# Optimization experiments

Hardware: AMD Instinct MI355X
Metric: run time of the kernel (lower is better)

## Reference

```python
import jax, jax.numpy as jnp
import numpy as np

B, T = 512, 512
VOCAB, EMB, DEC = 30001, 512, 128
MAX_OOVS = 50


def setup_inputs() -> dict:
    key = jax.random.key(0)
    ks = jax.random.split(key, 24)
    rn = lambda k, shp, s=0.05: (jax.random.normal(k, shp, dtype=jnp.float32) * s)
    emb = rn(ks[0], (VOCAB, EMB), 1.0).at[0].set(0.0)  # padding_idx=0
    return {
        'h_i': jax.random.normal(ks[1], (B, T, DEC), dtype=jnp.float32),
        'h_prev': jax.random.normal(ks[2], (B, DEC), dtype=jnp.float32),
        'c_prev': jax.random.normal(ks[3], (B, DEC), dtype=jnp.float32),
        'context_vector': jax.random.normal(ks[4], (B, DEC), dtype=jnp.float32),
        'coverage': jax.random.uniform(ks[5], (B, T), dtype=jnp.float32),
        'emb': emb,
        'W_ih': rn(ks[6], (4 * DEC, EMB)), 'W_hh': rn(ks[7], (4 * DEC, DEC)),
        'b_ih': rn(ks[8], (4 * DEC,)), 'b_hh': rn(ks[9], (4 * DEC,)),
        'W1_w': rn(ks[10], (EMB, EMB + DEC)), 'W1_b': rn(ks[11], (EMB,)),
        'W2_w': rn(ks[12], (1, 3 * DEC + EMB)), 'W2_b': rn(ks[13], (1,)),
        'V1_w': rn(ks[14], (3 * DEC, 2 * DEC)), 'V1_b': rn(ks[15], (3 * DEC,)),
        'V2_w': rn(ks[16], (VOCAB, 3 * DEC)), 'V2_b': rn(ks[17], (VOCAB,)),
        'Wh_w': rn(ks[18], (DEC, DEC)),
        'Ws_w': rn(ks[19], (DEC, 2 * DEC)), 'Ws_b': rn(ks[20], (DEC,)),
        'Wc_w': rn(ks[21], (DEC, 1)),
        'V_w': rn(ks[22], (1, DEC)),
        'x': jax.random.randint(ks[23], (B, 1), 0, VOCAB),
        'code_ext': jax.random.randint(jax.random.fold_in(key, 99), (B, T), 0, VOCAB + MAX_OOVS),
        'max_oovs': MAX_OOVS,
    }


def reference(h_i, h_prev, c_prev, context_vector, coverage, emb,
              W_ih, W_hh, b_ih, b_hh, W1_w, W1_b, W2_w, W2_b,
              V1_w, V1_b, V2_w, V2_b, Wh_w, Ws_w, Ws_b, Wc_w, V_w,
              x, code_ext, max_oovs):
    xe = emb[x[:, 0]]                                        # [B, EMB]
    x1 = jnp.concatenate([xe, context_vector], 1) @ W1_w.T + W1_b
    # LSTMCell (gate order i, f, g, o)
    gates = x1 @ W_ih.T + b_ih + h_prev @ W_hh.T + b_hh
    i, f, g, o = jnp.split(gates, 4, axis=1)
    c = jax.nn.sigmoid(f) * c_prev + jax.nn.sigmoid(i) * jnp.tanh(g)
    h = jax.nn.sigmoid(o) * jnp.tanh(c)
    s_t = jnp.concatenate([h, c], 1)                         # [B, 2*DEC]
    # Bahdanau attention with coverage
    enc_f = h_i @ Wh_w.T                                     # [B, T, DEC]
    dec_f = (s_t @ Ws_w.T + Ws_b)[:, None, :]
    cov_f = coverage[:, :, None] * Wc_w[:, 0][None, None, :]
    e_t = jnp.tanh(enc_f + dec_f + cov_f) @ V_w[0]           # [B, T]
    a_t = jax.nn.softmax(e_t, axis=-1)
    coverage_new = coverage + a_t
    ctx = jnp.einsum('bt,btd->bd', a_t, h_i)                 # [B, DEC]
    # vocab distribution
    pv = jnp.concatenate([h, ctx], 1) @ V1_w.T + V1_b
    pv = jax.nn.softmax(pv @ V2_w.T + V2_b, axis=1)          # [B, VOCAB]
    p_gen = jax.nn.sigmoid(jnp.concatenate([ctx, s_t, xe], 1) @ W2_w.T + W2_b)  # [B,1]
    pv = p_gen * pv
    attn_dist = (1.0 - p_gen) * a_t
    pv_ext = jnp.concatenate([pv, jnp.zeros((pv.shape[0], max_oovs), pv.dtype)], axis=-1)
    rows = jnp.arange(pv.shape[0])[:, None]
    final_dist = pv_ext.at[rows, code_ext].add(attn_dist)    # scatter_add copy mechanism
    return (final_dist, attn_dist, h, c, coverage_new, ctx)
```

## Files before the change

kernel.cpp:

```cpp
#include <hip/hip_runtime.h>
#include <math.h>

#define B_    512
#define T_    512
#define DEC_  128
#define EMB_  512
#define VOC_  30001
#define VEXT_ 30051

typedef float f32x4 __attribute__((ext_vector_type(4)));
typedef short s16x4 __attribute__((ext_vector_type(4)));
typedef short s16x8 __attribute__((ext_vector_type(8)));
typedef unsigned u32x4 __attribute__((ext_vector_type(4)));

#define L2E 1.4426950408889634f

__device__ __forceinline__ float sigmoid_f(float x) {
  return __builtin_amdgcn_rcpf(1.f + exp2f(-x * L2E));
}
__device__ __forceinline__ float tanh_f(float x) {
  return 1.f - 2.f * __builtin_amdgcn_rcpf(exp2f(x * (2.f * L2E)) + 1.f);
}
__device__ __forceinline__ short f2bf(float f) {
  unsigned u = __builtin_bit_cast(unsigned, f);
  u += 0x7FFFu + ((u >> 16) & 1u);
  return (short)(u >> 16);
}
__device__ __forceinline__ float bf2f(unsigned short h) {
  return __builtin_bit_cast(float, (unsigned)h << 16);
}
__device__ __forceinline__ float bitsf(unsigned u) {
  return __builtin_bit_cast(float, u);
}
__device__ __forceinline__ unsigned pk_bf16(float lo, float hi) {
  unsigned r;
  asm("v_cvt_pk_bf16_f32 %0, %1, %2" : "=v"(r) : "v"(lo), "v"(hi));
  return r;
}
__device__ __forceinline__ s16x8 pk8(f32x4 w0, f32x4 w1) {
  u32x4 r;
  r[0] = pk_bf16(w0[0], w0[1]); r[1] = pk_bf16(w0[2], w0[3]);
  r[2] = pk_bf16(w1[0], w1[1]); r[3] = pk_bf16(w1[2], w1[3]);
  return __builtin_bit_cast(s16x8, r);
}
__device__ __forceinline__ unsigned short* logit_row(float* outF, int b) {
  size_t byteoff = ((size_t)b * VEXT_ * 4 + 127) & ~(size_t)127;
  return (unsigned short*)((char*)outF + byteoff);
}
__device__ __forceinline__ void gload_lds16(const void* g, void* l) {
  __builtin_amdgcn_global_load_lds(
      (const __attribute__((address_space(1))) void*)g,
      (__attribute__((address_space(3))) void*)l, 16, 0, 0);
}

__global__ __launch_bounds__(256) void k0_prep32(
    const float* __restrict__ Whw, unsigned short* __restrict__ bw) {
  const int t = threadIdx.x;
#pragma unroll
  for (int i = 0; i < 8; ++i) {
    int p = t + 256 * i;
    int f = p >> 6, l = p & 63;
    int nf = f >> 2, kf = f & 3;
    int row = nf * 16 + (l & 15);
    int col = kf * 32 + (l >> 4) * 8;
    const float* src = Whw + row * 128 + col;
    f32x4 w0 = *(const f32x4*)src;
    f32x4 w1 = *(const f32x4*)(src + 4);
    *(s16x8*)&bw[p * 8] = pk8(w0, w1);
  }
}

__global__ __launch_bounds__(256) void k0b_prepv2h(
    const float* __restrict__ V2w, unsigned short* __restrict__ v2bh) {
  int p = blockIdx.x * 256 + threadIdx.x;
  int row = p / 48;
  int k = (p - row * 48) * 8;
  s16x8 bb;
  if (row < VOC_) {
    const float* src = V2w + (size_t)row * 384 + k;
    f32x4 w0 = *(const f32x4*)src;
    f32x4 w1 = *(const f32x4*)(src + 4);
    bb = pk8(w0, w1);
  } else {
    bb = (s16x8){0, 0, 0, 0, 0, 0, 0, 0};
  }
  *(s16x8*)&v2bh[(size_t)p * 8] = bb;
}

__global__ __launch_bounds__(256) void k0c_prepv1(
    const float* __restrict__ V1w, unsigned short* __restrict__ v1bh) {
  int p = blockIdx.x * 256 + threadIdx.x;
  int row = p >> 5, k = (p & 31) * 8;
  const float* src = V1w + row * 256 + k;
  *(s16x8*)&v1bh[p * 8] = pk8(*(const f32x4*)src, *(const f32x4*)(src + 4));
}

__global__ __launch_bounds__(256) void k1_x1(
    const float* __restrict__ emb, const int* __restrict__ x,
    const float* __restrict__ ctxp, const float* __restrict__ W1w,
    const float* __restrict__ W1b, float* __restrict__ x1) {
  __shared__ float As[32][33];
  __shared__ float Ws[32][33];
  const int tid = threadIdx.x;
  const int f0 = blockIdx.x * 32, b0 = blockIdx.y * 32;
  const int row = tid >> 3, seg = tid & 7;
  const int tx = tid & 15, ty = tid >> 4;
  float a00 = 0.f, a01 = 0.f, a10 = 0.f, a11 = 0.f;
  for (int k0 = 0; k0 < 640; k0 += 32) {
    int k = k0 + seg * 4;
    f32x4 av;
    if (k < 512) {
      int xb = x[b0 + row];
      av = *(const f32x4*)(emb + xb * 512 + k);
    } else {
      av = *(const f32x4*)(ctxp + (b0 + row) * 128 + (k - 512));
    }
    As[row][seg * 4 + 0] = av[0]; As[row][seg * 4 + 1] = av[1];
    As[row][seg * 4 + 2] = av[2]; As[row][seg * 4 + 3] = av[3];
    f32x4 wv = *(const f32x4*)(W1w + (f0 + row) * 640 + k);
    Ws[row][seg * 4 + 0] = wv[0]; Ws[row][seg * 4 + 1] = wv[1];
    Ws[row][seg * 4 + 2] = wv[2]; Ws[row][seg * 4 + 3] = wv[3];
    __syncthreads();
#pragma unroll
    for (int kk = 0; kk < 32; ++kk) {
      float v0 = As[ty * 2][kk], v1 = As[ty * 2 + 1][kk];
      float w0 = Ws[tx * 2][kk], w1 = Ws[tx * 2 + 1][kk];
      a00 += v0 * w0; a01 += v0 * w1; a10 += v1 * w0; a11 += v1 * w1;
    }
    __syncthreads();
  }
  int fo = f0 + tx * 2, bo = b0 + ty * 2;
  x1[bo * 512 + fo]           = a00 + W1b[fo];
  x1[bo * 512 + fo + 1]       = a01 + W1b[fo + 1];
  x1[(bo + 1) * 512 + fo]     = a10 + W1b[fo];
  x1[(bo + 1) * 512 + fo + 1] = a11 + W1b[fo + 1];
}

__global__ __launch_bounds__(256) void k2_gates(
    const float* __restrict__ x1, const float* __restrict__ hprev,
    const float* __restrict__ Wih, const float* __restrict__ Whh,
    const float* __restrict__ bih, const float* __restrict__ bhh,
    float* __restrict__ gates) {
  __shared__ float As[32][33];
  __shared__ float Ws[32][33];
  const int tid = threadIdx.x;
  const int f0 = blockIdx.x * 32, b0 = blockIdx.y * 32;
  const int row = tid >> 3, seg = tid & 7;
  const int tx = tid & 15, ty = tid >> 4;
  float a00 = 0.f, a01 = 0.f, a10 = 0.f, a11 = 0.f;
  for (int k0 = 0; k0 < 640; k0 += 32) {
    int k = k0 + seg * 4;
    f32x4 av, wv;
    if (k < 512) {
      av = *(const f32x4*)(x1 + (b0 + row) * 512 + k);
      wv = *(const f32x4*)(Wih + (f0 + row) * 512 + k);
    } else {
      av = *(const f32x4*)(hprev + (b0 + row) * 128 + (k - 512));
      wv = *(const f32x4*)(Whh + (f0 + row) * 128 + (k - 512));
    }
    As[row][seg * 4 + 0] = av[0]; As[row][seg * 4 + 1] = av[1];
    As[row][seg * 4 + 2] = av[2]; As[row][seg * 4 + 3] = av[3];
    Ws[row][seg * 4 + 0] = wv[0]; Ws[row][seg * 4 + 1] = wv[1];
    Ws[row][seg * 4 + 2] = wv[2]; Ws[row][seg * 4 + 3] = wv[3];
    __syncthreads();
#pragma unroll
    for (int kk = 0; kk < 32; ++kk) {
      float v0 = As[ty * 2][kk], v1 = As[ty * 2 + 1][kk];
      float w0 = Ws[tx * 2][kk], w1 = Ws[tx * 2 + 1][kk];
      a00 += v0 * w0; a01 += v0 * w1; a10 += v1 * w0; a11 += v1 * w1;
    }
    __syncthreads();
  }
  int fo = f0 + tx * 2, bo = b0 + ty * 2;
  gates[bo * 512 + fo]           = a00 + bih[fo] + bhh[fo];
  gates[bo * 512 + fo + 1]       = a01 + bih[fo + 1] + bhh[fo + 1];
  gates[(bo + 1) * 512 + fo]     = a10 + bih[fo] + bhh[fo];
  gates[(bo + 1) * 512 + fo + 1] = a11 + bih[fo + 1] + bhh[fo + 1];
}

__global__ __launch_bounds__(128) void k3_lstm(
    const float* __restrict__ gates, const float* __restrict__ cprev,
    const float* __restrict__ Wsw, const float* __restrict__ Wsb,
    float* __restrict__ out_h, float* __restrict__ out_c,
    float* __restrict__ decf, unsigned short* __restrict__ hc_bf) {
  __shared__ float st[256];
  int b = blockIdx.x, d = threadIdx.x;
  const float* g = gates + b * 512;
  float iv = sigmoid_f(g[d]);
  float fv = sigmoid_f(g[128 + d]);
  float gv = tanh_f(g[256 + d]);
  float ov = sigmoid_f(g[384 + d]);
  float c = fv * cprev[b * 128 + d] + iv * gv;
  float h = ov * tanh_f(c);
  out_h[b * 128 + d] = h;
  out_c[b * 128 + d] = c;
  hc_bf[b * 256 + d] = (unsigned short)f2bf(h);
  st[d] = h; st[128 + d] = c;
  __syncthreads();
  float acc = Wsb[d];
  const float* wr = Wsw + d * 256;
#pragma unroll 4
  for (int k = 0; k < 256; ++k) acc += st[k] * wr[k];
  decf[b * 128 + d] = acc;
}

__global__ __launch_bounds__(512) void k45_attn(
    const float* __restrict__ h_i, const unsigned short* __restrict__ bw,
    const float* __restrict__ decf, const float* __restrict__ cov,
    const float* __restrict__ Wcw, const float* __restrict__ Vw,
    float* __restrict__ a_t, float* __restrict__ cov_out,
    float* __restrict__ ctx_out, unsigned short* __restrict__ hc_bf) {
  __shared__ unsigned short whl[16384];
  __shared__ float sm[512];
  __shared__ float red[8][128];
  __shared__ float wred[8];
  __shared__ float dls[128], vls[128], wls[128];
  const int b = blockIdx.x;
  const int tid = threadIdx.x;
  const int wv = tid >> 6, lane = tid & 63;
  const int lm = lane & 15, lg = lane >> 4;
  const int t0w = wv * 64;

#pragma unroll
  for (int i = 0; i < 4; ++i)
    gload_lds16(&bw[(tid + i * 512) * 8], &whl[(tid + i * 512) * 8]);
  if (tid < 128) {
    dls[tid] = decf[b * 128 + tid];
    vls[tid] = Vw[tid];
    wls[tid] = Wcw[tid];
  }
  __syncthreads();

  const volatile float* vlp = vls;
  const volatile float* dlp = dls;
  const volatile float* wlp = wls;
  float E1 = 0.f;
#pragma unroll
  for (int nf = 0; nf < 8; ++nf) E1 += fabsf(vlp[nf * 16 + lm]);
  E1 += __shfl_xor(E1, 1); E1 += __shfl_xor(E1, 2);
  E1 += __shfl_xor(E1, 4); E1 += __shfl_xor(E1, 8);

  const f32x4 zf4 = {0.f, 0.f, 0.f, 0.f};
  const float* abase = h_i + ((size_t)(b * 512 + t0w + lm)) * 128 + lg * 8;

  f32x4 r0, r1, r2, r3, r4, r5, r6, r7;
  f32x4 cv_raw;
  f32x4 c0 = zf4, c1 = zf4, c2 = zf4, c3 = zf4;
  f32x4 c4 = zf4, c5 = zf4, c6 = zf4, c7 = zf4;
#define K45_LOADC(c)                                            \
  do {                                                          \
    const float* p_ = abase + (size_t)(c) * 16 * 128;           \
    r0 = *(const f32x4*)(p_ + 0);   r1 = *(const f32x4*)(p_ + 4);   \
    r2 = *(const f32x4*)(p_ + 32);  r3 = *(const f32x4*)(p_ + 36);  \
    r4 = *(const f32x4*)(p_ + 64);  r5 = *(const f32x4*)(p_ + 68);  \
    r6 = *(const f32x4*)(p_ + 96);  r7 = *(const f32x4*)(p_ + 100); \
    cv_raw = *(const f32x4*)&cov[b * 512 + t0w + (c) * 16 + lg * 4];\
  } while (0)
#define K45_ACC(ca, cb, pk)                                         \
  do {                                                              \
    u32x4 q_ = __builtin_bit_cast(u32x4, pk);                       \
    ca[0] += w * bitsf(q_[0] << 16); ca[1] += w * bitsf(q_[0] & 0xFFFF0000u); \
    ca[2] += w * bitsf(q_[1] << 16); ca[3] += w * bitsf(q_[1] & 0xFFFF0000u); \
    cb[0] += w * bitsf(q_[2] << 16); cb[1] += w * bitsf(q_[2] & 0xFFFF0000u); \
    cb[2] += w * bitsf(q_[3] << 16); cb[3] += w * bitsf(q_[3] & 0xFFFF0000u); \
  } while (0)

  K45_LOADC(0);
#pragma unroll
  for (int c = 0; c < 4; ++c) {
    s16x8 pk0 = pk8(r0, r1), pk1 = pk8(r2, r3);
    s16x8 pk2 = pk8(r4, r5), pk3 = pk8(r6, r7);
    f32x4 cov4 = cv_raw;
    if (c < 3) K45_LOADC(c + 1);

    float e4[4] = {0.f, 0.f, 0.f, 0.f};
#pragma unroll
    for (int nf = 0; nf < 8; ++nf) {
      float dv = dlp[nf * 16 + lm];
      float vw = vlp[nf * 16 + lm];
      float wc = wlp[nf * 16 + lm];
      s16x8 b0_ = *(const s16x8*)&whl[((nf * 4 + 0) * 64 + lane) * 8];
      s16x8 b1_ = *(const s16x8*)&whl[((nf * 4 + 1) * 64 + lane) * 8];
      s16x8 b2_ = *(const s16x8*)&whl[((nf * 4 + 2) * 64 + lane) * 8];
      s16x8 b3_ = *(const s16x8*)&whl[((nf * 4 + 3) * 64 + lane) * 8];
      f32x4 cc = zf4;
      cc = __builtin_amdgcn_mfma_f32_16x16x32_bf16(pk0, b0_, cc, 0, 0, 0);
      cc = __builtin_amdgcn_mfma_f32_16x16x32_bf16(pk1, b1_, cc, 0, 0, 0);
      cc = __builtin_amdgcn_mfma_f32_16x16x32_bf16(pk2, b2_, cc, 0, 0, 0);
      cc = __builtin_amdgcn_mfma_f32_16x16x32_bf16(pk3, b3_, cc, 0, 0, 0);
#pragma unroll
      for (int r = 0; r < 4; ++r) {
        float v = cc[r] + dv + cov4[r] * wc;
        e4[r] += vw * tanh_f(v);
      }
    }
#pragma unroll
    for (int i = 0; i < 4; ++i) {
      float v = e4[i];
      v += __shfl_xor(v, 1); v += __shfl_xor(v, 2);
      v += __shfl_xor(v, 4); v += __shfl_xor(v, 8);
      e4[i] = v;
    }
    if (lm == 0) {
#pragma unroll
      for (int r = 0; r < 4; ++r)
        sm[t0w + c * 16 + lg * 4 + r] = e4[r];
    }
    int src = (lm >> 2) << 4;
    float s0 = __shfl(e4[0], src), s1 = __shfl(e4[1], src);
    float s2 = __shfl(e4[2], src), s3 = __shfl(e4[3], src);
    int rr = lm & 3;
    float ev = rr == 0 ? s0 : (rr == 1 ? s1 : (rr == 2 ? s2 : s3));
    float w = exp2f((ev - E1) * L2E);
    K45_ACC(c0, c1, pk0);
    K45_ACC(c2, c3, pk1);
    K45_ACC(c4, c5, pk2);
    K45_ACC(c6, c7, pk3);
  }
#undef K45_LOADC
#undef K45_ACC

#define BFLY(x) { x += __shfl_xor(x, 1); x += __shfl_xor(x, 2); \
                  x += __shfl_xor(x, 4); x += __shfl_xor(x, 8); }
#pragma unroll
  for (int j = 0; j < 4; ++j) {
    BFLY(c0[j]); BFLY(c1[j]); BFLY(c2[j]); BFLY(c3[j]);
    BFLY(c4[j]); BFLY(c5[j]); BFLY(c6[j]); BFLY(c7[j]);
  }
#undef BFLY
  if (lm == 0) {
    float* rw = &red[wv][lg * 8];
#pragma unroll
    for (int j = 0; j < 4; ++j) {
      rw[j] = c0[j];       rw[4 + j] = c1[j];
      rw[32 + j] = c2[j];  rw[36 + j] = c3[j];
      rw[64 + j] = c4[j];  rw[68 + j] = c5[j];
      rw[96 + j] = c6[j];  rw[100 + j] = c7[j];
    }
  }
  __syncthreads();

  float e = sm[tid];
  float w2 = exp2f((e - E1) * L2E);
  float s = w2;
  for (int off = 32; off; off >>= 1) s += __shfl_xor(s, off);
  if (lane == 0) wred[wv] = s;
  __syncthreads();
  float S1 = 0.f;
#pragma unroll
  for (int i = 0; i < 8; ++i) S1 += wred[i];
  float rS = __builtin_amdgcn_rcpf(S1);
  float a = w2 * rS;
  a_t[b * 512 + tid] = a;
  cov_out[b * 512 + tid] = cov[b * 512 + tid] + a;
  if (tid < 128) {
    float sa = 0.f;
#pragma unroll
    for (int g = 0; g < 8; ++g) sa += red[g][tid];
    float cx = sa * rS;
    ctx_out[b * 128 + tid] = cx;
    hc_bf[b * 256 + 128 + tid] = (unsigned short)f2bf(cx);
  }
}

__global__ __launch_bounds__(256) void k6a_pv1(
    const unsigned short* __restrict__ hc_bf, const unsigned short* __restrict__ v1bh,
    const float* __restrict__ V1b, unsigned short* __restrict__ pv1bf) {
  __shared__ char smem[33280];
  unsigned short* Al = (unsigned short*)smem;
  unsigned short* Bl = (unsigned short*)(smem + 16384);
  const int bx = blockIdx.x;
  const int rp = bx & 3, cp = bx >> 2;
  const int r0 = rp * 128, c0 = cp * 128;
  const int tid = threadIdx.x;
  const int wv = tid >> 6, lane = tid & 63;
  const int lm = lane & 15, lg = lane >> 4;
  const int rh2 = wv >> 1, ch = wv & 1;

  const f32x4 zf4 = {0.f, 0.f, 0.f, 0.f};
  f32x4 acc[4][4];
#pragma unroll
  for (int m = 0; m < 4; ++m)
#pragma unroll
    for (int nf = 0; nf < 4; ++nf) acc[m][nf] = zf4;

  for (int ks = 0; ks < 4; ++ks) {
#pragma unroll
    for (int i = 0; i < 4; ++i) {
      int fi = wv * 4 + i;
      int rt = fi >> 1, kf = fi & 1;
      const unsigned short* sa =
          hc_bf + (r0 + rt * 16 + lm) * 256 + ks * 64 + kf * 32 + lg * 8;
      gload_lds16(sa, &Al[fi * 512 + lane * 8]);
      const unsigned short* sb =
          v1bh + (c0 + rt * 16 + lm) * 256 + ks * 64 + kf * 32 + lg * 8;
      gload_lds16(sb, &Bl[fi * 512 + lane * 8]);
    }
    __syncthreads();
#pragma unroll
    for (int kf = 0; kf < 2; ++kf) {
      s16x8 a[4];
#pragma unroll
      for (int m = 0; m < 4; ++m)
        a[m] = *(const s16x8*)&Al[(((rh2 * 4 + m) * 2) + kf) * 512 + lane * 8];
#pragma unroll
      for (int nf = 0; nf < 4; ++nf) {
        s16x8 bfr = *(const s16x8*)&Bl[(((ch * 4 + nf) * 2) + kf) * 512 + lane * 8];
#pragma unroll
        for (int m = 0; m < 4; ++m)
          acc[m][nf] = __builtin_amdgcn_mfma_f32_16x16x32_bf16(a[m], bfr, acc[m][nf], 0, 0, 0);
      }
    }
    __syncthreads();
  }

  const int cw0 = c0 + ch * 64;
  float bias[4];
#pragma unroll
  for (int nf = 0; nf < 4; ++nf)
    bias[nf] = V1b[cw0 + nf * 16 + lm];

  float* T = (float*)smem + wv * 2080;
  const int rq = lane >> 4, cq = lane & 15;
#pragma unroll
  for (int p = 0; p < 2; ++p) {
#pragma unroll
    for (int mm = 0; mm < 2; ++mm) {
      int m = p * 2 + mm;
#pragma unroll
      for (int nf = 0; nf < 4; ++nf)
#pragma unroll
        for (int r = 0; r < 4; ++r)
          T[(mm * 16 + lg * 4 + r) * 65 + nf * 16 + lm] = acc[m][nf][r] + bias[nf];
    }
#pragma unroll
    for (int it = 0; it < 8; ++it) {
      int trow = it * 4 + rq;
      f32x4 vv = *(const f32x4*)&T[trow * 65 + cq * 4];
      s16x4 hb;
      hb[0] = f2bf(vv[0]); hb[1] = f2bf(vv[1]); hb[2] = f2bf(vv[2]); hb[3] = f2bf(vv[3]);
      int orow = r0 + rh2 * 64 + p * 32 + trow;
      *(s16x4*)&pv1bf[orow * 384 + cw0 + cq * 4] = hb;
    }
  }
}

__global__ __launch_bounds__(256) void k6b_pgen(
    const float* __restrict__ out_h, const float* __restrict__ out_c,
    const float* __restrict__ ctx, const float* __restrict__ emb,
    const int* __restrict__ x, const float* __restrict__ W2w,
    const float* __restrict__ W2b, const float* __restrict__ a_t,
    float* __restrict__ pgen, float* __restrict__ attn_out) {
  __shared__ float cat[896];
  __shared__ float wr_[4];
  int b = blockIdx.x, tid = threadIdx.x;
  if (tid < 128) {
    cat[tid] = ctx[b * 128 + tid];
    cat[128 + tid] = out_h[b * 128 + tid];
  } else {
    int q = tid - 128;
    cat[256 + q] = out_c[b * 128 + q];
  }
  int xb = x[b];
  for (int k = tid; k < 512; k += 256) cat[384 + k] = emb[xb * 512 + k];
  __syncthreads();
  float p = 0.f;
  for (int k = tid; k < 896; k += 256) p += cat[k] * W2w[k];
  for (int off = 32; off; off >>= 1) p += __shfl_xor(p, off);
  if ((tid & 63) == 0) wr_[tid >> 6] = p;
  __syncthreads();
  float pg = sigmoid_f(wr_[0] + wr_[1] + wr_[2] + wr_[3] + W2b[0]);
  if (tid == 0) pgen[b] = pg;
  float om = 1.f - pg;
  attn_out[b * 512 + tid]       = om * a_t[b * 512 + tid];
  attn_out[b * 512 + 256 + tid] = om * a_t[b * 512 + 256 + tid];
}

__global__ __launch_bounds__(256) void k7_vocab(
    const unsigned short* __restrict__ pv1bf, const unsigned short* __restrict__ v2bh,
    const float* __restrict__ V2b, float* __restrict__ outF) {
  __shared__ char smem[33280];
  unsigned short* Al = (unsigned short*)smem;
  unsigned short* Bl = (unsigned short*)(smem + 16384);
  const int bx = blockIdx.x;
  const int rp = bx & 3, cp = bx >> 2;
  const int r0 = rp * 128, c0 = cp * 128;
  const int tid = threadIdx.x;
  const int wv = tid >> 6, lane = tid & 63;
  const int lm = lane & 15, lg = lane >> 4;
  const int rh2 = wv >> 1, ch = wv & 1;

  const f32x4 zf4 = {0.f, 0.f, 0.f, 0.f};
  f32x4 acc[4][4];
#pragma unroll
  for (int m = 0; m < 4; ++m)
#pragma unroll
    for (int nf = 0; nf < 4; ++nf) acc[m][nf] = zf4;

  for (int ks = 0; ks < 6; ++ks) {
#pragma unroll
    for (int i = 0; i < 4; ++i) {
      int fi = wv * 4 + i;
      int rt = fi >> 1, kf = fi & 1;
      const unsigned short* sa =
          pv1bf + (r0 + rt * 16 + lm) * 384 + ks * 64 + kf * 32 + lg * 8;
      gload_lds16(sa, &Al[fi * 512 + lane * 8]);
      const unsigned short* sb =
          v2bh + (size_t)(c0 + rt * 16 + lm) * 384 + ks * 64 + kf * 32 + lg * 8;
      gload_lds16(sb, &Bl[fi * 512 + lane * 8]);
    }
    __syncthreads();
#pragma unroll
    for (int kf = 0; kf < 2; ++kf) {
      s16x8 a[4];
#pragma unroll
      for (int m = 0; m < 4; ++m)
        a[m] = *(const s16x8*)&Al[(((rh2 * 4 + m) * 2) + kf) * 512 + lane * 8];
#pragma unroll
      for (int nf = 0; nf < 4; ++nf) {
        s16x8 bfr = *(const s16x8*)&Bl[(((ch * 4 + nf) * 2) + kf) * 512 + lane * 8];
#pragma unroll
        for (int m = 0; m < 4; ++m)
          acc[m][nf] = __builtin_amdgcn_mfma_f32_16x16x32_bf16(a[m], bfr, acc[m][nf], 0, 0, 0);
      }
    }
    __syncthreads();
  }

  const int cw0 = c0 + ch * 64;
  float bias[4];
#pragma unroll
  for (int nf = 0; nf < 4; ++nf) {
    int col = cw0 + nf * 16 + lm;
    bias[nf] = (col < VOC_) ? V2b[col] : 0.f;
  }

  float* T = (float*)smem + wv * 2080;
  const int rq = lane >> 4, cq = lane & 15;
#pragma unroll
  for (int p = 0; p < 2; ++p) {
#pragma unroll
    for (int mm = 0; mm < 2; ++mm) {
      int m = p * 2 + mm;
#pragma unroll
      for (int nf = 0; nf < 4; ++nf)
#pragma unroll
        for (int r = 0; r < 4; ++r)
          T[(mm * 16 + lg * 4 + r) * 65 + nf * 16 + lm] = acc[m][nf][r] + bias[nf];
    }
#pragma unroll
    for (int it = 0; it < 8; ++it) {
      int trow = it * 4 + rq;
      f32x4 vv = *(const f32x4*)&T[trow * 65 + cq * 4];
      s16x4 hb;
      hb[0] = f2bf(vv[0]); hb[1] = f2bf(vv[1]); hb[2] = f2bf(vv[2]); hb[3] = f2bf(vv[3]);
      int orow = r0 + rh2 * 64 + p * 32 + trow;
      unsigned short* dst = logit_row(outF, orow);
      *(s16x4*)&dst[cw0 + cq * 4] = hb;
    }
  }
}

__global__ __launch_bounds__(256) void k7_vocab_fb(
    const unsigned short* __restrict__ pv1bf, const float* __restrict__ V2w,
    const float* __restrict__ V2b, float* __restrict__ outF) {
  __shared__ float lt[4][32 * 65];
  const int q = blockIdx.x;
  const int nb = ((q >> 4) << 3) + (q & 7);
  const int rh = (q >> 3) & 1;
  if (nb >= 469) return;
  const int v0 = nb * 64;
  const int tid = threadIdx.x;
  const int wv = tid >> 6, lane = tid & 63;
  const int lm = lane & 15, lg = lane >> 4;
  const int r0 = rh * 256 + wv * 64;

  const f32x4 zf4 = {0.f, 0.f, 0.f, 0.f};
  f32x4 acc[4][4];
#pragma unroll
  for (int m = 0; m < 4; ++m)
#pragma unroll
    for (int nf = 0; nf < 4; ++nf) acc[m][nf] = zf4;

  int vrow[4]; bool vok[4];
#pragma unroll
  for (int nf = 0; nf < 4; ++nf) {
    int v = v0 + nf * 16 + lm;
    vok[nf] = (v < VOC_);
    vrow[nf] = vok[nf] ? v : (VOC_ - 1);
  }

#pragma unroll
  for (int kf = 0; kf < 12; ++kf) {
    s16x8 afr[4];
#pragma unroll
    for (int m = 0; m < 4; ++m)
      afr[m] = *(const s16x8*)&pv1bf[(r0 + m * 16 + lm) * 384 + kf * 32 + lg * 8];
    s16x8 bfr[4];
#pragma unroll
    for (int nf = 0; nf < 4; ++nf) {
      const float* p = V2w + (size_t)vrow[nf] * 384 + kf * 32 + lg * 8;
      f32x4 w0 = *(const f32x4*)p;
      f32x4 w1 = *(const f32x4*)(p + 4);
      if (!vok[nf]) { w0 = zf4; w1 = zf4; }
      bfr[nf] = pk8(w0, w1);
    }
#pragma unroll
    for (int m = 0; m < 4; ++m)
#pragma unroll
      for (int nf = 0; nf < 4; ++nf)
        acc[m][nf] = __builtin_amdgcn_mfma_f32_16x16x32_bf16(afr[m], bfr[nf], acc[m][nf], 0, 0, 0);
  }

  float bias[4];
#pragma unroll
  for (int nf = 0; nf < 4; ++nf)
    bias[nf] = vok[nf] ? V2b[v0 + nf * 16 + lm] : 0.f;

  float* T = lt[wv];
  const int rq = lane >> 4, cq = lane & 15;
#pragma unroll
  for (int p = 0; p < 2; ++p) {
#pragma unroll
    for (int mm = 0; mm < 2; ++mm) {
      int m = p * 2 + mm;
#pragma unroll
      for (int nf = 0; nf < 4; ++nf)
#pragma unroll
        for (int r = 0; r < 4; ++r)
          T[(mm * 16 + lg * 4 + r) * 65 + nf * 16 + lm] = acc[m][nf][r] + bias[nf];
    }
#pragma unroll
    for (int it = 0; it < 8; ++it) {
      int trow = it * 4 + rq;
      f32x4 vv = *(const f32x4*)&T[trow * 65 + cq * 4];
      s16x4 hb;
      hb[0] = f2bf(vv[0]); hb[1] = f2bf(vv[1]); hb[2] = f2bf(vv[2]); hb[3] = f2bf(vv[3]);
      int orow = r0 + p * 32 + trow;
      unsigned short* dst = logit_row(outF, orow);
      *(s16x4*)&dst[v0 + cq * 4] = hb;
    }
  }
}

#define K8_IT 30

__global__ __launch_bounds__(1024) void k8_final(
    const float* __restrict__ pgen, const int* __restrict__ code_ext,
    const float* __restrict__ attn, float* __restrict__ outF) {
  __shared__ float lm_[16], ls_[16];
  const int b = blockIdx.x, tid = threadIdx.x;
  float* row = outF + (size_t)b * VEXT_;
  const unsigned short* lrow = logit_row(outF, b);

  float lv[K8_IT];
#pragma unroll
  for (int i = 0; i < K8_IT; ++i) {
    int v = tid + i * 1024;
    lv[i] = (v < VOC_) ? bf2f(lrow[v]) : -3.4e38f;
  }
  float m = lv[0];
#pragma unroll
  for (int i = 1; i < K8_IT; ++i) m = fmaxf(m, lv[i]);
  for (int off = 32; off; off >>= 1) m = fmaxf(m, __shfl_xor(m, off));
  if ((tid & 63) == 0) lm_[tid >> 6] = m;
  __syncthreads();
  float M = lm_[0];
#pragma unroll
  for (int i = 1; i < 16; ++i) M = fmaxf(M, lm_[i]);
  float s = 0.f;
#pragma unroll
  for (int i = 0; i < K8_IT; ++i) {
    lv[i] = exp2f((lv[i] - M) * L2E);
    s += lv[i];
  }
  for (int off = 32; off; off >>= 1) s += __shfl_xor(s, off);
  if ((tid & 63) == 0) ls_[tid >> 6] = s;
  __syncthreads();
  float S = 0.f;
#pragma unroll
  for (int i = 0; i < 16; ++i) S += ls_[i];
  float pm = pgen[b] / S;
#pragma unroll
  for (int i = 0; i < K8_IT; ++i) {
    int v = tid + i * 1024;
    if (v < VOC_) row[v] = pm * lv[i];
  }
  if (tid < 50) row[VOC_ + tid] = 0.f;
  __syncthreads();
  if (tid < 512) {
    int idx = code_ext[b * 512 + tid];
    __hip_atomic_fetch_add(&row[idx], attn[b * 512 + tid],
                           __ATOMIC_RELAXED, __HIP_MEMORY_SCOPE_WORKGROUP);
  }
}

extern "C" void kernel_launch(void* const* d_in, const int* in_sizes, int n_in,
                              void* d_out, int out_size, void* d_ws, size_t ws_size,
                              hipStream_t stream) {
  (void)in_sizes; (void)n_in; (void)out_size;
  const float* h_i    = (const float*)d_in[0];
  const float* h_prev = (const float*)d_in[1];
  const float* c_prev = (const float*)d_in[2];
  const float* ctxp   = (const float*)d_in[3];
  const float* cov    = (const float*)d_in[4];
  const float* emb    = (const float*)d_in[5];
  const float* Wih    = (const float*)d_in[6];
  const float* Whh    = (const float*)d_in[7];
  const float* bih    = (const float*)d_in[8];
  const float* bhh    = (const float*)d_in[9];
  const float* W1w    = (const float*)d_in[10];
  const float* W1b    = (const float*)d_in[11];
  const float* W2w    = (const float*)d_in[12];
  const float* W2b    = (const float*)d_in[13];
  const float* V1w    = (const float*)d_in[14];
  const float* V1b    = (const float*)d_in[15];
  const float* V2w    = (const float*)d_in[16];
  const float* V2b    = (const float*)d_in[17];
  const float* Whw    = (const float*)d_in[18];
  const float* Wsw    = (const float*)d_in[19];
  const float* Wsb    = (const float*)d_in[20];
  const float* Wcw    = (const float*)d_in[21];
  const float* Vw     = (const float*)d_in[22];
  const int*   x      = (const int*)d_in[23];
  const int*   code   = (const int*)d_in[24];

  float* ws    = (float*)d_ws;
  float* x1    = ws;
  float* gates = ws + 262144;
  float* decf  = ws + 524288;
  unsigned short* bw = (unsigned short*)(ws + 589824);
  unsigned short* hc_bf = (unsigned short*)(ws + 598016);
  unsigned short* v1bh  = (unsigned short*)(ws + 663552);
  float* a_t   = ws + 851968;
  unsigned short* pv1bf = (unsigned short*)(ws + 1114112);
  float* pgen  = ws + 1212416;
  unsigned short* v2bh = (unsigned short*)(ws + 1212928);
  const size_t WS_NEEDED = (size_t)(1212928 + 5775360) * 4;
  const bool use_v6 = (ws_size >= WS_NEEDED);

  float* outF  = (float*)d_out;
  float* attn  = outF + (size_t)512 * VEXT_;
  float* o_h   = attn + 262144;
  float* o_c   = o_h + 65536;
  float* o_cov = o_c + 65536;
  float* o_ctx = o_cov + 262144;

  k0_prep32<<<1, 256, 0, stream>>>(Whw, bw);
  if (use_v6) k0b_prepv2h<<<5640, 256, 0, stream>>>(V2w, v2bh);
  k0c_prepv1<<<48, 256, 0, stream>>>(V1w, v1bh);
  k1_x1<<<dim3(16, 16), 256, 0, stream>>>(emb, x, ctxp, W1w, W1b, x1);
  k2_gates<<<dim3(16, 16), 256, 0, stream>>>(x1, h_prev, Wih, Whh, bih, bhh, gates);
  k3_lstm<<<512, 128, 0, stream>>>(gates, c_prev, Wsw, Wsb, o_h, o_c, decf, hc_bf);
  k45_attn<<<512, 512, 0, stream>>>(h_i, bw, decf, cov, Wcw, Vw, a_t, o_cov,
                                    o_ctx, hc_bf);
  k6a_pv1<<<12, 256, 0, stream>>>(hc_bf, v1bh, V1b, pv1bf);
  k6b_pgen<<<512, 256, 0, stream>>>(o_h, o_c, o_ctx, emb, x, W2w, W2b, a_t,
                                    pgen, attn);
  if (use_v6)
    k7_vocab<<<940, 256, 0, stream>>>(pv1bf, v2bh, V2b, outF);
  else
    k7_vocab_fb<<<944, 256, 0, stream>>>(pv1bf, V2w, V2b, outF);
  k8_final<<<512, 1024, 0, stream>>>(pgen, code, attn, outF);
}
```

Baseline: 221.7 us.

## Split attention over two blocks per batch row and merge in pgen kernel

The attention kernel now launches two blocks per batch row, each covering half of the 512 timesteps. Each block writes unnormalized exp weights, a partial context sum and a partial softmax denominator. A new merge kernel, fused with the p_gen computation, combines the two halves, normalizes, and writes ctx, coverage, attn_dist and the bf16 context. The goal is twice as many blocks for the bandwidth-heavy h_i pass, at the cost of an extra round-trip of partial results through global memory and the attention→pv1 dependency now passing through the merge kernel. The fixed max shift E1 keeps the two halves on a common scale without a second pass.

```diff
diff --git a/kernel.cpp b/kernel.cpp
--- a/kernel.cpp
+++ b/kernel.cpp
@@ -208,18 +208,19 @@
     const float* __restrict__ h_i, const unsigned short* __restrict__ bw,
     const float* __restrict__ decf, const float* __restrict__ cov,
     const float* __restrict__ Wcw, const float* __restrict__ Vw,
-    float* __restrict__ a_t, float* __restrict__ cov_out,
-    float* __restrict__ ctx_out, unsigned short* __restrict__ hc_bf) {
+    float* __restrict__ wbuf, float* __restrict__ cxp,
+    float* __restrict__ Sp) {
   __shared__ unsigned short whl[16384];
-  __shared__ float sm[512];
+  __shared__ float sm[256];
   __shared__ float red[8][128];
   __shared__ float wred[8];
   __shared__ float dls[128], vls[128], wls[128];
-  const int b = blockIdx.x;
+  const int bx = blockIdx.x;
+  const int b = bx >> 1, g = bx & 1;
   const int tid = threadIdx.x;
   const int wv = tid >> 6, lane = tid & 63;
   const int lm = lane & 15, lg = lane >> 4;
-  const int t0w = wv * 64;
+  const int t0w = g * 256 + wv * 32;
 
 #pragma unroll
   for (int i = 0; i < 4; ++i)
@@ -267,11 +268,11 @@
 
   K45_LOADC(0);
 #pragma unroll
-  for (int c = 0; c < 4; ++c) {
+  for (int c = 0; c < 2; ++c) {
     s16x8 pk0 = pk8(r0, r1), pk1 = pk8(r2, r3);
     s16x8 pk2 = pk8(r4, r5), pk3 = pk8(r6, r7);
     f32x4 cov4 = cv_raw;
-    if (c < 3) K45_LOADC(c + 1);
+    if (c < 1) K45_LOADC(c + 1);
 
     float e4[4] = {0.f, 0.f, 0.f, 0.f};
 #pragma unroll
@@ -304,7 +305,7 @@
     if (lm == 0) {
 #pragma unroll
       for (int r = 0; r < 4; ++r)
-        sm[t0w + c * 16 + lg * 4 + r] = e4[r];
+        sm[wv * 32 + c * 16 + lg * 4 + r] = e4[r];
     }
     int src = (lm >> 2) << 4;
     float s0 = __shfl(e4[0], src), s1 = __shfl(e4[1], src);
@@ -340,27 +341,65 @@
   }
   __syncthreads();
 
-  float e = sm[tid];
-  float w2 = exp2f((e - E1) * L2E);
-  float s = w2;
-  for (int off = 32; off; off >>= 1) s += __shfl_xor(s, off);
-  if (lane == 0) wred[wv] = s;
-  __syncthreads();
-  float S1 = 0.f;
-#pragma unroll
-  for (int i = 0; i < 8; ++i) S1 += wred[i];
-  float rS = __builtin_amdgcn_rcpf(S1);
-  float a = w2 * rS;
-  a_t[b * 512 + tid] = a;
-  cov_out[b * 512 + tid] = cov[b * 512 + tid] + a;
   if (tid < 128) {
     float sa = 0.f;
 #pragma unroll
-    for (int g = 0; g < 8; ++g) sa += red[g][tid];
-    float cx = sa * rS;
+    for (int q = 0; q < 8; ++q) sa += red[q][tid];
+    cxp[(size_t)bx * 128 + tid] = sa;
+  }
+  if (tid < 256) {
+    float e = sm[tid];
+    float w2 = exp2f((e - E1) * L2E);
+    wbuf[b * 512 + g * 256 + tid] = w2;
+    float s = w2;
+    for (int off = 32; off; off >>= 1) s += __shfl_xor(s, off);
+    if (lane == 0) wred[wv] = s;
+  }
+  __syncthreads();
+  if (tid == 0) Sp[bx] = wred[0] + wred[1] + wred[2] + wred[3];
+}
+
+__global__ __launch_bounds__(256) void k6b_merge(
+    const float* __restrict__ out_h, const float* __restrict__ out_c,
+    const float* __restrict__ emb, const int* __restrict__ x,
+    const float* __restrict__ W2w, const float* __restrict__ W2b,
+    const float* __restrict__ cov, const float* __restrict__ wbuf,
+    const float* __restrict__ cxp, const float* __restrict__ Sp,
+    float* __restrict__ pgen, float* __restrict__ attn_out,
+    float* __restrict__ cov_out, float* __restrict__ ctx_out,
+    unsigned short* __restrict__ hc_bf) {
+  __shared__ float cat[896];
+  __shared__ float wr_[4];
+  int b = blockIdx.x, tid = threadIdx.x;
+  float rS = __builtin_amdgcn_rcpf(Sp[2 * b] + Sp[2 * b + 1]);
+  if (tid < 128) {
+    float cx = (cxp[(size_t)(2 * b) * 128 + tid] +
+                cxp[(size_t)(2 * b + 1) * 128 + tid]) * rS;
     ctx_out[b * 128 + tid] = cx;
     hc_bf[b * 256 + 128 + tid] = (unsigned short)f2bf(cx);
-  }
+    cat[tid] = cx;
+    cat[128 + tid] = out_h[b * 128 + tid];
+  } else {
+    int q = tid - 128;
+    cat[256 + q] = out_c[b * 128 + q];
+  }
+  int xb = x[b];
+  for (int k = tid; k < 512; k += 256) cat[384 + k] = emb[xb * 512 + k];
+  __syncthreads();
+  float p = 0.f;
+  for (int k = tid; k < 896; k += 256) p += cat[k] * W2w[k];
+  for (int off = 32; off; off >>= 1) p += __shfl_xor(p, off);
+  if ((tid & 63) == 0) wr_[tid >> 6] = p;
+  __syncthreads();
+  float pg = sigmoid_f(wr_[0] + wr_[1] + wr_[2] + wr_[3] + W2b[0]);
+  if (tid == 0) pgen[b] = pg;
+  float om = 1.f - pg;
+  float w0 = wbuf[b * 512 + tid], w1 = wbuf[b * 512 + 256 + tid];
+  float a0 = w0 * rS, a1 = w1 * rS;
+  cov_out[b * 512 + tid]       = cov[b * 512 + tid] + a0;
+  cov_out[b * 512 + 256 + tid] = cov[b * 512 + 256 + tid] + a1;
+  attn_out[b * 512 + tid]       = om * a0;
+  attn_out[b * 512 + 256 + tid] = om * a1;
 }
 
 __global__ __launch_bounds__(256) void k6a_pv1(
@@ -443,37 +482,6 @@
       *(s16x4*)&pv1bf[orow * 384 + cw0 + cq * 4] = hb;
     }
   }
-}
-
-__global__ __launch_bounds__(256) void k6b_pgen(
-    const float* __restrict__ out_h, const float* __restrict__ out_c,
-    const float* __restrict__ ctx, const float* __restrict__ emb,
-    const int* __restrict__ x, const float* __restrict__ W2w,
-    const float* __restrict__ W2b, const float* __restrict__ a_t,
-    float* __restrict__ pgen, float* __restrict__ attn_out) {
-  __shared__ float cat[896];
-  __shared__ float wr_[4];
-  int b = blockIdx.x, tid = threadIdx.x;
-  if (tid < 128) {
-    cat[tid] = ctx[b * 128 + tid];
-    cat[128 + tid] = out_h[b * 128 + tid];
-  } else {
-    int q = tid - 128;
-    cat[256 + q] = out_c[b * 128 + q];
-  }
-  int xb = x[b];
-  for (int k = tid; k < 512; k += 256) cat[384 + k] = emb[xb * 512 + k];
-  __syncthreads();
-  float p = 0.f;
-  for (int k = tid; k < 896; k += 256) p += cat[k] * W2w[k];
-  for (int off = 32; off; off >>= 1) p += __shfl_xor(p, off);
-  if ((tid & 63) == 0) wr_[tid >> 6] = p;
-  __syncthreads();
-  float pg = sigmoid_f(wr_[0] + wr_[1] + wr_[2] + wr_[3] + W2b[0]);
-  if (tid == 0) pgen[b] = pg;
-  float om = 1.f - pg;
-  attn_out[b * 512 + tid]       = om * a_t[b * 512 + tid];
-  attn_out[b * 512 + 256 + tid] = om * a_t[b * 512 + 256 + tid];
 }
 
 __global__ __launch_bounds__(256) void k7_vocab(
@@ -727,12 +735,14 @@
 
   float* ws    = (float*)d_ws;
   float* x1    = ws;
+  float* cxp   = ws;
+  float* Sp    = ws + 131072;
   float* gates = ws + 262144;
   float* decf  = ws + 524288;
   unsigned short* bw = (unsigned short*)(ws + 589824);
   unsigned short* hc_bf = (unsigned short*)(ws + 598016);
   unsigned short* v1bh  = (unsigned short*)(ws + 663552);
-  float* a_t   = ws + 851968;
+  float* wbuf  = ws + 851968;
   unsigned short* pv1bf = (unsigned short*)(ws + 1114112);
   float* pgen  = ws + 1212416;
   unsigned short* v2bh = (unsigned short*)(ws + 1212928);
@@ -752,11 +762,10 @@
   k1_x1<<<dim3(16, 16), 256, 0, stream>>>(emb, x, ctxp, W1w, W1b, x1);
   k2_gates<<<dim3(16, 16), 256, 0, stream>>>(x1, h_prev, Wih, Whh, bih, bhh, gates);
   k3_lstm<<<512, 128, 0, stream>>>(gates, c_prev, Wsw, Wsb, o_h, o_c, decf, hc_bf);
-  k45_attn<<<512, 512, 0, stream>>>(h_i, bw, decf, cov, Wcw, Vw, a_t, o_cov,
-                                    o_ctx, hc_bf);
+  k45_attn<<<1024, 512, 0, stream>>>(h_i, bw, decf, cov, Wcw, Vw, wbuf, cxp, Sp);
+  k6b_merge<<<512, 256, 0, stream>>>(o_h, o_c, emb, x, W2w, W2b, cov, wbuf,
+                                     cxp, Sp, pgen, attn, o_cov, o_ctx, hc_bf);
   k6a_pv1<<<12, 256, 0, stream>>>(hc_bf, v1bh, V1b, pv1bf);
-  k6b_pgen<<<512, 256, 0, stream>>>(o_h, o_c, o_ctx, emb, x, W2w, W2b, a_t,
-                                    pgen, attn);
   if (use_v6)
     k7_vocab<<<940, 256, 0, stream>>>(pv1bf, v2bh, V2b, outF);
   else
```

After: 235.9 us. 1.06x slower.

## Replace fp32 SIMT x1/gates GEMMs with bf16 MFMA kernels and a prep pass

Applied to the files above, without the earlier changes.

A new prep kernel converts the gathered embedding and context input, h_prev, W1 and the concatenated W_ih/W_hh to bf16 in row-major layouts. The two fp32 shared-memory GEMMs then become 128x128-tile bf16 MFMA kernels that load global memory directly into LDS. The first GEMM writes x1 as bf16 straight into the second GEMM's concatenated input buffer, which removes the separate fp32 x1 round trip. In exchange it adds an extra launch and runs only 16 blocks per GEMM, and bf16 rounding of x1 and the weights lowers precision.

```diff
diff --git a/kernel.cpp b/kernel.cpp
--- a/kernel.cpp
+++ b/kernel.cpp
@@ -95,87 +95,201 @@
   *(s16x8*)&v1bh[p * 8] = pk8(*(const f32x4*)src, *(const f32x4*)(src + 4));
 }
 
-__global__ __launch_bounds__(256) void k1_x1(
+__global__ __launch_bounds__(256) void k0d_prep12(
     const float* __restrict__ emb, const int* __restrict__ x,
-    const float* __restrict__ ctxp, const float* __restrict__ W1w,
-    const float* __restrict__ W1b, float* __restrict__ x1) {
-  __shared__ float As[32][33];
-  __shared__ float Ws[32][33];
+    const float* __restrict__ ctxp, const float* __restrict__ hprev,
+    const float* __restrict__ W1w, const float* __restrict__ Wih,
+    const float* __restrict__ Whh,
+    unsigned short* __restrict__ abuf, unsigned short* __restrict__ a2buf,
+    unsigned short* __restrict__ w1b, unsigned short* __restrict__ w2b) {
+  int g = blockIdx.x * 256 + threadIdx.x;
+  const float* src;
+  unsigned short* dst;
+  if (g < 40960) {
+    int idx = g * 8, b = idx / 640, k = idx - b * 640;
+    src = (k < 512) ? emb + (size_t)x[b] * 512 + k : ctxp + b * 128 + (k - 512);
+    dst = abuf + idx;
+  } else if (g < 49152) {
+    int q = (g - 40960) * 8, b = q >> 7, d = q & 127;
+    src = hprev + b * 128 + d;
+    dst = a2buf + b * 640 + 512 + d;
+  } else if (g < 90112) {
+    int idx = (g - 49152) * 8;
+    src = W1w + idx;
+    dst = w1b + idx;
+  } else {
+    int idx = (g - 90112) * 8, f = idx / 640, k = idx - f * 640;
+    src = (k < 512) ? Wih + f * 512 + k : Whh + f * 128 + (k - 512);
+    dst = w2b + idx;
+  }
+  f32x4 w0 = *(const f32x4*)src;
+  f32x4 w1 = *(const f32x4*)(src + 4);
+  *(s16x8*)&dst[0] = pk8(w0, w1);
+}
+
+__global__ __launch_bounds__(256) void k1mm(
+    const unsigned short* __restrict__ abuf, const unsigned short* __restrict__ w1b,
+    const float* __restrict__ W1b, unsigned short* __restrict__ a2buf) {
+  __shared__ char smem[33280];
+  unsigned short* Al = (unsigned short*)smem;
+  unsigned short* Bl = (unsigned short*)(smem + 16384);
+  const int bx = blockIdx.x;
+  const int rp = bx & 3, cp = bx >> 2;
+  const int r0 = rp * 128, c0 = cp * 128;
   const int tid = threadIdx.x;
-  const int f0 = blockIdx.x * 32, b0 = blockIdx.y * 32;
-  const int row = tid >> 3, seg = tid & 7;
-  const int tx = tid & 15, ty = tid >> 4;
-  float a00 = 0.f, a01 = 0.f, a10 = 0.f, a11 = 0.f;
-  for (int k0 = 0; k0 < 640; k0 += 32) {
-    int k = k0 + seg * 4;
-    f32x4 av;
-    if (k < 512) {
-      int xb = x[b0 + row];
-      av = *(const f32x4*)(emb + xb * 512 + k);
-    } else {
-      av = *(const f32x4*)(ctxp + (b0 + row) * 128 + (k - 512));
-    }
-    As[row][seg * 4 + 0] = av[0]; As[row][seg * 4 + 1] = av[1];
-    As[row][seg * 4 + 2] = av[2]; As[row][seg * 4 + 3] = av[3];
-    f32x4 wv = *(const f32x4*)(W1w + (f0 + row) * 640 + k);
-    Ws[row][seg * 4 + 0] = wv[0]; Ws[row][seg * 4 + 1] = wv[1];
-    Ws[row][seg * 4 + 2] = wv[2]; Ws[row][seg * 4 + 3] = wv[3];
+  const int wv = tid >> 6, lane = tid & 63;
+  const int lm = lane & 15, lg = lane >> 4;
+  const int rh2 = wv >> 1, ch = wv & 1;
+
+  const f32x4 zf4 = {0.f, 0.f, 0.f, 0.f};
+  f32x4 acc[4][4];
+#pragma unroll
+  for (int m = 0; m < 4; ++m)
+#pragma unroll
+    for (int nf = 0; nf < 4; ++nf) acc[m][nf] = zf4;
+
+  for (int ks = 0; ks < 10; ++ks) {
+#pragma unroll
+    for (int i = 0; i < 4; ++i) {
+      int fi = wv * 4 + i;
+      int rt = fi >> 1, kf = fi & 1;
+      const unsigned short* sa =
+          abuf + (r0 + rt * 16 + lm) * 640 + ks * 64 + kf * 32 + lg * 8;
+      gload_lds16(sa, &Al[fi * 512 + lane * 8]);
+      const unsigned short* sb =
+          w1b + (c0 + rt * 16 + lm) * 640 + ks * 64 + kf * 32 + lg * 8;
+      gload_lds16(sb, &Bl[fi * 512 + lane * 8]);
+    }
     __syncthreads();
 #pragma unroll
-    for (int kk = 0; kk < 32; ++kk) {
-      float v0 = As[ty * 2][kk], v1 = As[ty * 2 + 1][kk];
-      float w0 = Ws[tx * 2][kk], w1 = Ws[tx * 2 + 1][kk];
-      a00 += v0 * w0; a01 += v0 * w1; a10 += v1 * w0; a11 += v1 * w1;
+    for (int kf = 0; kf < 2; ++kf) {
+      s16x8 a[4];
+#pragma unroll
+      for (int m = 0; m < 4; ++m)
+        a[m] = *(const s16x8*)&Al[(((rh2 * 4 + m) * 2) + kf) * 512 + lane * 8];
+#pragma unroll
+      for (int nf = 0; nf < 4; ++nf) {
+        s16x8 bfr = *(const s16x8*)&Bl[(((ch * 4 + nf) * 2) + kf) * 512 + lane * 8];
+#pragma unroll
+        for (int m = 0; m < 4; ++m)
+          acc[m][nf] = __builtin_amdgcn_mfma_f32_16x16x32_bf16(a[m], bfr, acc[m][nf], 0, 0, 0);
+      }
     }
     __syncthreads();
   }
-  int fo = f0 + tx * 2, bo = b0 + ty * 2;
-  x1[bo * 512 + fo]           = a00 + W1b[fo];
-  x1[bo * 512 + fo + 1]       = a01 + W1b[fo + 1];
-  x1[(bo + 1) * 512 + fo]     = a10 + W1b[fo];
-  x1[(bo + 1) * 512 + fo + 1] = a11 + W1b[fo + 1];
-}
-
-__global__ __launch_bounds__(256) void k2_gates(
-    const float* __restrict__ x1, const float* __restrict__ hprev,
-    const float* __restrict__ Wih, const float* __restrict__ Whh,
+
+  const int cw0 = c0 + ch * 64;
+  float bias[4];
+#pragma unroll
+  for (int nf = 0; nf < 4; ++nf)
+    bias[nf] = W1b[cw0 + nf * 16 + lm];
+
+  float* T = (float*)smem + wv * 2080;
+  const int rq = lane >> 4, cq = lane & 15;
+#pragma unroll
+  for (int p = 0; p < 2; ++p) {
+#pragma unroll
+    for (int mm = 0; mm < 2; ++mm) {
+      int m = p * 2 + mm;
+#pragma unroll
+      for (int nf = 0; nf < 4; ++nf)
+#pragma unroll
+        for (int r = 0; r < 4; ++r)
+          T[(mm * 16 + lg * 4 + r) * 65 + nf * 16 + lm] = acc[m][nf][r] + bias[nf];
+    }
+#pragma unroll
+    for (int it = 0; it < 8; ++it) {
+      int trow = it * 4 + rq;
+      f32x4 vv = *(const f32x4*)&T[trow * 65 + cq * 4];
+      s16x4 hb;
+      hb[0] = f2bf(vv[0]); hb[1] = f2bf(vv[1]); hb[2] = f2bf(vv[2]); hb[3] = f2bf(vv[3]);
+      int orow = r0 + rh2 * 64 + p * 32 + trow;
+      *(s16x4*)&a2buf[orow * 640 + cw0 + cq * 4] = hb;
+    }
+  }
+}
+
+__global__ __launch_bounds__(256) void k2mm(
+    const unsigned short* __restrict__ a2buf, const unsigned short* __restrict__ w2b,
     const float* __restrict__ bih, const float* __restrict__ bhh,
     float* __restrict__ gates) {
-  __shared__ float As[32][33];
-  __shared__ float Ws[32][33];
+  __shared__ char smem[33280];
+  unsigned short* Al = (unsigned short*)smem;
+  unsigned short* Bl = (unsigned short*)(smem + 16384);
+  const int bx = blockIdx.x;
+  const int rp = bx & 3, cp = bx >> 2;
+  const int r0 = rp * 128, c0 = cp * 128;
   const int tid = threadIdx.x;
-  const int f0 = blockIdx.x * 32, b0 = blockIdx.y * 32;
-  const int row = tid >> 3, seg = tid & 7;
-  const int tx = tid & 15, ty = tid >> 4;
-  float a00 = 0.f, a01 = 0.f, a10 = 0.f, a11 = 0.f;
-  for (int k0 = 0; k0 < 640; k0 += 32) {
-    int k = k0 + seg * 4;
-    f32x4 av, wv;
-    if (k < 512) {
-      av = *(const f32x4*)(x1 + (b0 + row) * 512 + k);
-      wv = *(const f32x4*)(Wih + (f0 + row) * 512 + k);
-    } else {
-      av = *(const f32x4*)(hprev + (b0 + row) * 128 + (k - 512));
-      wv = *(const f32x4*)(Whh + (f0 + row) * 128 + (k - 512));
-    }
-    As[row][seg * 4 + 0] = av[0]; As[row][seg * 4 + 1] = av[1];
-    As[row][seg * 4 + 2] = av[2]; As[row][seg * 4 + 3] = av[3];
-    Ws[row][seg * 4 + 0] = wv[0]; Ws[row][seg * 4 + 1] = wv[1];
-    Ws[row][seg * 4 + 2] = wv[2]; Ws[row][seg * 4 + 3] = wv[3];
+  const int wv = tid >> 6, lane = tid & 63;
+  const int lm = lane & 15, lg = lane >> 4;
+  const int rh2 = wv >> 1, ch = wv & 1;
+
+  const f32x4 zf4 = {0.f, 0.f, 0.f, 0.f};
+  f32x4 acc[4][4];
+#pragma unroll
+  for (int m = 0; m < 4; ++m)
+#pragma unroll
+    for (int nf = 0; nf < 4; ++nf) acc[m][nf] = zf4;
+
+  for (int ks = 0; ks < 10; ++ks) {
+#pragma unroll
+    for (int i = 0; i < 4; ++i) {
+      int fi = wv * 4 + i;
+      int rt = fi >> 1, kf = fi & 1;
+      const unsigned short* sa =
+          a2buf + (r0 + rt * 16 + lm) * 640 + ks * 64 + kf * 32 + lg * 8;
+      gload_lds16(sa, &Al[fi * 512 + lane * 8]);
+      const unsigned short* sb =
+          w2b + (c0 + rt * 16 + lm) * 640 + ks * 64 + kf * 32 + lg * 8;
+      gload_lds16(sb, &Bl[fi * 512 + lane * 8]);
+    }
     __syncthreads();
 #pragma unroll
-    for (int kk = 0; kk < 32; ++kk) {
-      float v0 = As[ty * 2][kk], v1 = As[ty * 2 + 1][kk];
-      float w0 = Ws[tx * 2][kk], w1 = Ws[tx * 2 + 1][kk];
-      a00 += v0 * w0; a01 += v0 * w1; a10 += v1 * w0; a11 += v1 * w1;
+    for (int kf = 0; kf < 2; ++kf) {
+      s16x8 a[4];
+#pragma unroll
+      for (int m = 0; m < 4; ++m)
+        a[m] = *(const s16x8*)&Al[(((rh2 * 4 + m) * 2) + kf) * 512 + lane * 8];
+#pragma unroll
+      for (int nf = 0; nf < 4; ++nf) {
+        s16x8 bfr = *(const s16x8*)&Bl[(((ch * 4 + nf) * 2) + kf) * 512 + lane * 8];
+#pragma unroll
+        for (int m = 0; m < 4; ++m)
+          acc[m][nf] = __builtin_amdgcn_mfma_f32_16x16x32_bf16(a[m], bfr, acc[m][nf], 0, 0, 0);
+      }
     }
     __syncthreads();
   }
-  int fo = f0 + tx * 2, bo = b0 + ty * 2;
-  gates[bo * 512 + fo]           = a00 + bih[fo] + bhh[fo];
-  gates[bo * 512 + fo + 1]       = a01 + bih[fo + 1] + bhh[fo + 1];
-  gates[(bo + 1) * 512 + fo]     = a10 + bih[fo] + bhh[fo];
-  gates[(bo + 1) * 512 + fo + 1] = a11 + bih[fo + 1] + bhh[fo + 1];
+
+  const int cw0 = c0 + ch * 64;
+  float bias[4];
+#pragma unroll
+  for (int nf = 0; nf < 4; ++nf) {
+    int col = cw0 + nf * 16 + lm;
+    bias[nf] = bih[col] + bhh[col];
+  }
+
+  float* T = (float*)smem + wv * 2080;
+  const int rq = lane >> 4, cq = lane & 15;
+#pragma unroll
+  for (int p = 0; p < 2; ++p) {
+#pragma unroll
+    for (int mm = 0; mm < 2; ++mm) {
+      int m = p * 2 + mm;
+#pragma unroll
+      for (int nf = 0; nf < 4; ++nf)
+#pragma unroll
+        for (int r = 0; r < 4; ++r)
+          T[(mm * 16 + lg * 4 + r) * 65 + nf * 16 + lm] = acc[m][nf][r] + bias[nf];
+    }
+#pragma unroll
+    for (int it = 0; it < 8; ++it) {
+      int trow = it * 4 + rq;
+      f32x4 vv = *(const f32x4*)&T[trow * 65 + cq * 4];
+      int orow = r0 + rh2 * 64 + p * 32 + trow;
+      *(f32x4*)&gates[(size_t)orow * 512 + cw0 + cq * 4] = vv;
+    }
+  }
 }
 
 __global__ __launch_bounds__(128) void k3_lstm(
@@ -725,13 +839,16 @@
   const int*   x      = (const int*)d_in[23];
   const int*   code   = (const int*)d_in[24];
 
-  float* ws    = (float*)d_ws;
-  float* x1    = ws;
-  float* gates = ws + 262144;
-  float* decf  = ws + 524288;
-  unsigned short* bw = (unsigned short*)(ws + 589824);
-  unsigned short* hc_bf = (unsigned short*)(ws + 598016);
-  unsigned short* v1bh  = (unsigned short*)(ws + 663552);
+  float* ws = (float*)d_ws;
+  unsigned short* abuf  = (unsigned short*)(ws);
+  unsigned short* a2buf = (unsigned short*)(ws + 163840);
+  float* gates = ws + 327680;
+  float* decf  = ws + 589824;
+  unsigned short* bw    = (unsigned short*)(ws + 655360);
+  unsigned short* hc_bf = (unsigned short*)(ws + 663552);
+  unsigned short* v1bh  = (unsigned short*)(ws + 729088);
+  unsigned short* w1b   = (unsigned short*)(ws + 778240);
+  unsigned short* w2b   = (unsigned short*)(ws + 942080);
   float* a_t   = ws + 851968;
   unsigned short* pv1bf = (unsigned short*)(ws + 1114112);
   float* pgen  = ws + 1212416;
@@ -749,8 +866,10 @@
   k0_prep32<<<1, 256, 0, stream>>>(Whw, bw);
   if (use_v6) k0b_prepv2h<<<5640, 256, 0, stream>>>(V2w, v2bh);
   k0c_prepv1<<<48, 256, 0, stream>>>(V1w, v1bh);
-  k1_x1<<<dim3(16, 16), 256, 0, stream>>>(emb, x, ctxp, W1w, W1b, x1);
-  k2_gates<<<dim3(16, 16), 256, 0, stream>>>(x1, h_prev, Wih, Whh, bih, bhh, gates);
+  k0d_prep12<<<512, 256, 0, stream>>>(emb, x, ctxp, h_prev, W1w, Wih, Whh,
+                                      abuf, a2buf, w1b, w2b);
+  k1mm<<<16, 256, 0, stream>>>(abuf, w1b, W1b, a2buf);
+  k2mm<<<16, 256, 0, stream>>>(a2buf, w2b, bih, bhh, gates);
   k3_lstm<<<512, 128, 0, stream>>>(gates, c_prev, Wsw, Wsb, o_h, o_c, decf, hc_bf);
   k45_attn<<<512, 512, 0, stream>>>(h_i, bw, decf, cov, Wcw, Vw, a_t, o_cov,
                                     o_ctx, hc_bf);
```

Result: faster. 211.3 us (-4.7%).
